# Performance work log

Hardware: AMD Instinct MI355X
Metric: run time of the kernel (lower is better)

## Reference

```python
import jax, jax.numpy as jnp
import numpy as np

SKIP = 2 ** -0.5
EPS = 1e-6
DIM = 1024
N_LAYERS = 8
N_HEADS = 16
MAX_SEQ = 1024
B = 4
L = 1024


def get_rot_emb(dim, max_seq_len):
    pos = jnp.arange(max_seq_len, dtype=jnp.float32)
    omega = 1.0 / 10000.0 ** (jnp.arange(0, dim, 2, dtype=jnp.float32) / dim)
    angles = pos[:, None] * omega[None, :]  # [S, dim/2]
    cos = jnp.repeat(jnp.cos(angles), 2, axis=-1)  # [S, dim]
    sin = jnp.repeat(jnp.sin(angles), 2, axis=-1)
    return cos, sin


def setup_inputs() -> dict:
    key = jax.random.key(0)
    ks = jax.random.split(key, 16)
    s = 0.02
    d = DIM
    nl = N_LAYERS
    cos, sin = get_rot_emb(d // N_HEADS, MAX_SEQ)
    inp = {
        'x': jax.random.normal(ks[0], (B, L, d), jnp.float32),
        'c': jax.random.normal(ks[1], (B, 1, d), jnp.float32),
        't': jax.random.normal(ks[2], (B, d), jnp.float32),
        'num_heads': N_HEADS,
        'cos': cos,
        'sin': sin,
        'qkv_w': jax.random.normal(ks[3], (nl, d, 3 * d), jnp.float32) * s,
        'qkv_b': jnp.zeros((nl, 3 * d), jnp.float32),
        'proj_w': jax.random.normal(ks[4], (nl, d, d), jnp.float32) * s,
        'proj_b': jnp.zeros((nl, d), jnp.float32),
        'mlp_w1': jax.random.normal(ks[5], (nl, d, 4 * d), jnp.float32) * s,
        'mlp_b1': jnp.zeros((nl, 4 * d), jnp.float32),
        'mlp_w2': jax.random.normal(ks[6], (nl, 4 * d, d), jnp.float32) * s,
        'mlp_b2': jnp.zeros((nl, d), jnp.float32),
        'adaln_w': jax.random.normal(ks[7], (nl, d, 6 * d), jnp.float32) * s,
        'adaln_b': jnp.zeros((nl, 6 * d), jnp.float32),
    }
    return inp


def layer_norm(x):
    mu = jnp.mean(x, axis=-1, keepdims=True)
    var = jnp.var(x, axis=-1, keepdims=True)
    return (x - mu) * jax.lax.rsqrt(var + EPS)


def rotate_half(q):
    # torch: stack([-q[..., 1::2], q[..., ::2]], -1).reshape(q.shape)
    q2 = q.reshape(q.shape[:-1] + (-1, 2))
    return jnp.stack([-q2[..., 1], q2[..., 0]], axis=-1).reshape(q.shape)


def reference(x, c, t, num_heads, cos, sin, qkv_w, qkv_b, proj_w, proj_b, mlp_w1, mlp_b1, mlp_w2, mlp_b2, adaln_w, adaln_b):
    Bx, Lx, C = x.shape
    H = int(num_heads)
    D = C // H
    scale = D ** -0.5
    cmod = (c + t[:, None]) * SKIP  # [B,1,C]
    cos_l = cos[:Lx]  # [L,D]
    sin_l = sin[:Lx]

    def block(xcur, p):
        qw, qb, pw, pb, w1, b1, w2, b2, aw, ab = p
        mod = jax.nn.silu(cmod) @ aw + ab  # [B,1,6C]
        sh1, sc1, g1, sh2, sc2, g2 = jnp.split(mod, 6, axis=-1)
        h = (layer_norm(xcur) * (1 + sc1) + sh1) * SKIP
        qkv = (h @ qw + qb).reshape(Bx, Lx, 3, H, D).transpose(2, 0, 3, 1, 4)
        q, k, v = qkv[0], qkv[1], qkv[2]  # [B,H,L,D]
        q = q * cos_l + rotate_half(q) * sin_l
        k = k * cos_l + rotate_half(k) * sin_l
        attn = jax.nn.softmax(scale * jnp.einsum('bhid,bhjd->bhij', q, k), axis=-1)
        o = jnp.einsum('bhij,bhjd->bhid', attn, v).transpose(0, 2, 1, 3).reshape(Bx, Lx, C)
        o = o @ pw + pb
        xcur = (xcur + g1 * o) * SKIP
        h2 = (layer_norm(xcur) * (1 + sc2) + sh2) * SKIP
        m = jax.nn.gelu(h2 @ w1 + b1, approximate=True) @ w2 + b2
        return (xcur + g2 * m) * SKIP, None

    params = (qkv_w, qkv_b, proj_w, proj_b, mlp_w1, mlp_b1, mlp_w2, mlp_b2, adaln_w, adaln_b)
    out, _ = jax.lax.scan(block, x, params)
    return out
```

## Files before the change

kernel.cpp:

```cpp
#include <hip/hip_runtime.h>

#define SKIPF 0.70710678118654752440f

typedef unsigned short u16;
typedef unsigned int u32;
typedef __attribute__((ext_vector_type(4))) short bf16x4;
typedef __attribute__((ext_vector_type(8))) short bf16x8;
typedef __attribute__((ext_vector_type(4))) float f32x4;

#define MFMA32(A, B, C) __builtin_amdgcn_mfma_f32_16x16x32_bf16(A, B, C, 0, 0, 0)
#define MFMA16(A, B, C) __builtin_amdgcn_mfma_f32_16x16x16bf16_1k(A, B, C, 0, 0, 0)

__device__ __forceinline__ float bf2f(u16 v) {
  u32 u = ((u32)v) << 16; float f; __builtin_memcpy(&f, &u, 4); return f;
}
__device__ __forceinline__ u16 f2bf(float f) {
  u32 u; __builtin_memcpy(&u, &f, 4);
  u = (u + 0x7fffu + ((u >> 16) & 1u)) >> 16;
  return (u16)u;
}
__device__ __forceinline__ u32 cvtpk(float a, float b) {
  u32 r;
  asm("v_cvt_pk_bf16_f32 %0, %1, %2" : "=v"(r) : "v"(a), "v"(b));
  return r;
}
__device__ __forceinline__ void gload16(const void* g, void* s) {
  __builtin_amdgcn_global_load_lds((const __attribute__((address_space(1))) void*)g,
                                   (__attribute__((address_space(3))) void*)s, 16, 0, 0);
}

__global__ __launch_bounds__(256) void adaln_part_kernel(const float* __restrict__ c,
                                                         const float* __restrict__ t,
                                                         const float* __restrict__ aw,
                                                         float* __restrict__ part) {
  __shared__ float sc[4][32];
  int n = blockIdx.x * 256 + threadIdx.x;
  int ks = blockIdx.y;
  int k0 = ks * 32;
  if (threadIdx.x < 128) {
    int b = threadIdx.x >> 5, kk = threadIdx.x & 31;
    float xx = (c[b * 1024 + k0 + kk] + t[b * 1024 + k0 + kk]) * SKIPF;
    sc[b][kk] = xx / (1.f + __expf(-xx));
  }
  __syncthreads();
  float a0 = 0.f, a1 = 0.f, a2 = 0.f, a3 = 0.f;
#pragma unroll 4
  for (int k = 0; k < 32; ++k) {
    float w = aw[(size_t)(k0 + k) * 6144 + n];
    a0 += sc[0][k] * w; a1 += sc[1][k] * w; a2 += sc[2][k] * w; a3 += sc[3][k] * w;
  }
  part[(size_t)(ks * 4 + 0) * 6144 + n] = a0;
  part[(size_t)(ks * 4 + 1) * 6144 + n] = a1;
  part[(size_t)(ks * 4 + 2) * 6144 + n] = a2;
  part[(size_t)(ks * 4 + 3) * 6144 + n] = a3;
}

__global__ void adaln_reduce_kernel(const float* __restrict__ part, const float* __restrict__ ab,
                                    float* __restrict__ mod) {
  int i = blockIdx.x * 256 + threadIdx.x;
  int b = i / 6144, n = i - b * 6144;
  float a = ab[n];
#pragma unroll 4
  for (int ks = 0; ks < 32; ++ks) a += part[(size_t)(ks * 4 + b) * 6144 + n];
  mod[(size_t)b * 6144 + n] = a;
}

__global__ void wtrans4_kernel(const float* __restrict__ wq, u16* __restrict__ oq,
                               const float* __restrict__ wp, u16* __restrict__ op,
                               const float* __restrict__ w1p, u16* __restrict__ o1,
                               const float* __restrict__ w2p, u16* __restrict__ o2) {
  __shared__ float tile[32][33];
  int bid = blockIdx.x;
  const float* W; u16* WT; int nx, K, N, base;
  if (bid < 3072)      { W = wq;  WT = oq; nx = 96;  K = 1024; N = 3072; base = 0; }
  else if (bid < 4096) { W = wp;  WT = op; nx = 32;  K = 1024; N = 1024; base = 3072; }
  else if (bid < 8192) { W = w1p; WT = o1; nx = 128; K = 1024; N = 4096; base = 4096; }
  else                 { W = w2p; WT = o2; nx = 32;  K = 4096; N = 1024; base = 8192; }
  int t = bid - base;
  int n0 = (t % nx) * 32, k0 = (t / nx) * 32;
  int tx = threadIdx.x, ty = threadIdx.y;
#pragma unroll
  for (int i = 0; i < 4; ++i)
    tile[ty * 4 + i][tx] = W[(size_t)(k0 + ty * 4 + i) * N + n0 + tx];
  __syncthreads();
#pragma unroll
  for (int i = 0; i < 4; ++i)
    WT[(size_t)(n0 + ty * 4 + i) * K + k0 + tx] = f2bf(tile[tx][ty * 4 + i]);
}

__global__ __launch_bounds__(256) void ln_mod_kernel(const float* __restrict__ xin,
                                                     const float* __restrict__ mod,
                                                     u16* __restrict__ h, int sh_off, int sc_off) {
  int row = blockIdx.x;
  int b = row >> 10;
  const float4* xr = (const float4*)(xin + (size_t)row * 1024);
  float4 v = xr[threadIdx.x];
  float s = v.x + v.y + v.z + v.w;
  float ss = v.x * v.x + v.y * v.y + v.z * v.z + v.w * v.w;
#pragma unroll
  for (int o = 32; o; o >>= 1) { s += __shfl_xor(s, o); ss += __shfl_xor(ss, o); }
  __shared__ float red[8];
  int wave = threadIdx.x >> 6;
  if ((threadIdx.x & 63) == 0) { red[wave * 2] = s; red[wave * 2 + 1] = ss; }
  __syncthreads();
  s = red[0] + red[2] + red[4] + red[6];
  ss = red[1] + red[3] + red[5] + red[7];
  float mu = s * (1.f / 1024.f);
  float var = ss * (1.f / 1024.f) - mu * mu;
  float rs = rsqrtf(var + 1e-6f);
  int n = threadIdx.x * 4;
  const float* mb = mod + (size_t)b * 6144;
  float4 sc = *(const float4*)(mb + sc_off + n);
  float4 sh = *(const float4*)(mb + sh_off + n);
  ushort4 o4;
  o4.x = f2bf(((v.x - mu) * rs * (1.f + sc.x) + sh.x) * SKIPF);
  o4.y = f2bf(((v.y - mu) * rs * (1.f + sc.y) + sh.y) * SKIPF);
  o4.z = f2bf(((v.z - mu) * rs * (1.f + sc.z) + sh.z) * SKIPF);
  o4.w = f2bf(((v.w - mu) * rs * (1.f + sc.w) + sh.w) * SKIPF);
  *(ushort4*)(h + (size_t)row * 1024 + n) = o4;
}

template <int EPI>
__global__ __launch_bounds__(512, 1) void gemm256r_kernel(
    const u16* __restrict__ A, const u16* __restrict__ BT, const float* __restrict__ bias,
    u16* __restrict__ Cb, int NBX, int N, int K) {
  __shared__ u16 lds[4][16384];
  const int tid = threadIdx.x;
  const int lane = tid & 63, wave = tid >> 6;
  const int lq = lane & 15, lk = lane >> 4;
  const int wr = wave >> 2, wc = wave & 3;

  int per = gridDim.x >> 3;
  int swz = (blockIdx.x & 7) * per + (blockIdx.x >> 3);
  int bx = swz % NBX, by = swz / NBX;
  const int m0 = by * 256, n0 = bx * 256;

  f32x4 acc[8][4];
#pragma unroll
  for (int i = 0; i < 8; ++i)
#pragma unroll
    for (int j = 0; j < 4; ++j) acc[i][j] = (f32x4){0.f, 0.f, 0.f, 0.f};

  auto STAGE = [&](int slot, int t) {
    int kt = t * 32;
    char* Ab = (char*)lds[slot];
    char* Bb = (char*)(lds[slot] + 8192);
#pragma unroll
    for (int q = 0; q < 2; ++q) {
      int u = tid + q * 512;
      int r = u >> 3, cpos = u & 7;
      int g = cpos ^ (r & 7);
      gload16(A + (size_t)(m0 + 2 * r + (g >> 2)) * K + kt + (g & 3) * 8, Ab + u * 16);
    }
#pragma unroll
    for (int q = 0; q < 2; ++q) {
      int u = tid + q * 512;
      int r = u >> 3, cpos = u & 7;
      int g = cpos ^ (r & 7);
      gload16(BT + (size_t)(n0 + 2 * r + (g >> 2)) * K + kt + (g & 3) * 8, Bb + u * 16);
    }
  };

  const int NT = K >> 5;
  STAGE(0, 0); STAGE(1, 1); STAGE(2, 2);
  int slot = 0;
  for (int t = 0; t < NT; ++t) {
    int rem = NT - 1 - t;
    if (rem >= 2) asm volatile("s_waitcnt vmcnt(8)" ::: "memory");
    else if (rem == 1) asm volatile("s_waitcnt vmcnt(4)" ::: "memory");
    else asm volatile("s_waitcnt vmcnt(0)" ::: "memory");
    __builtin_amdgcn_s_barrier();
    __builtin_amdgcn_sched_barrier(0);
    if (t + 3 < NT) { int ns = slot + 3; if (ns >= 4) ns -= 4; STAGE(ns, t + 3); }
    const char* Ab = (const char*)lds[slot];
    const char* Bb = (const char*)(lds[slot] + 8192);
    bf16x8 bfr[4];
#pragma unroll
    for (int ni = 0; ni < 4; ++ni) {
      int nrow = wc * 64 + ni * 16 + lq;
      int r = nrow >> 1, g = (nrow & 1) * 4 + lk;
      bfr[ni] = *(const bf16x8*)(Bb + r * 128 + ((g ^ (r & 7)) << 4));
    }
#pragma unroll
    for (int ph = 0; ph < 4; ++ph) {
      bf16x8 af0, af1;
      {
        int mrow = wr * 128 + (ph * 2) * 16 + lq;
        int r = mrow >> 1, g = (mrow & 1) * 4 + lk;
        af0 = *(const bf16x8*)(Ab + r * 128 + ((g ^ (r & 7)) << 4));
        mrow += 16;
        r = mrow >> 1; g = (mrow & 1) * 4 + lk;
        af1 = *(const bf16x8*)(Ab + r * 128 + ((g ^ (r & 7)) << 4));
      }
      __builtin_amdgcn_s_setprio(1);
#pragma unroll
      for (int j = 0; j < 4; ++j) acc[ph * 2][j] = MFMA32(af0, bfr[j], acc[ph * 2][j]);
#pragma unroll
      for (int j = 0; j < 4; ++j) acc[ph * 2 + 1][j] = MFMA32(af1, bfr[j], acc[ph * 2 + 1][j]);
      __builtin_amdgcn_s_setprio(0);
    }
    ++slot; if (slot >= 4) slot = 0;
  }

#pragma unroll
  for (int i = 0; i < 8; ++i) {
    int rbase = m0 + wr * 128 + i * 16 + lk * 4;
#pragma unroll
    for (int j = 0; j < 4; ++j) {
      int cg = n0 + wc * 64 + j * 16 + lq;
      float bv = bias[cg];
#pragma unroll
      for (int r = 0; r < 4; ++r) {
        int row = rbase + r;
        float val = acc[i][j][r] + bv;
        if (EPI == 0) {
          Cb[(size_t)row * N + cg] = f2bf(val);
        } else {
          float tt = 0.7978845608028654f * (val + 0.044715f * val * val * val);
          float e = __expf(2.f * tt);
          float th = 1.f - 2.f / (e + 1.f);
          Cb[(size_t)row * N + cg] = f2bf(0.5f * val * (1.f + th));
        }
      }
    }
  }
}

__global__ __launch_bounds__(256) void gemm_res128_kernel(
    const u16* __restrict__ A, const u16* __restrict__ BT, const float* __restrict__ bias,
    const float* __restrict__ xin, float* __restrict__ xout, const float* __restrict__ mod,
    int g_off, int K) {
  __shared__ u16 lds[3][8192];
  const int tid = threadIdx.x;
  const int lane = tid & 63, wave = tid >> 6;
  const int lq = lane & 15, lk = lane >> 4;
  const int wr = wave >> 1, wc = wave & 1;
  const int m0 = blockIdx.x * 128, n0 = blockIdx.y * 128;

  f32x4 acc[4][4];
#pragma unroll
  for (int i = 0; i < 4; ++i)
#pragma unroll
    for (int j = 0; j < 4; ++j) acc[i][j] = (f32x4){0.f, 0.f, 0.f, 0.f};

  auto STAGE = [&](int slot, int t) {
    int kt = t * 32;
    char* Ab = (char*)lds[slot];
    char* Bb = (char*)(lds[slot] + 4096);
#pragma unroll
    for (int q = 0; q < 2; ++q) {
      int u = tid + q * 256;
      int r = u >> 3, cpos = u & 7;
      int g = cpos ^ (r & 7);
      gload16(A + (size_t)(m0 + 2 * r + (g >> 2)) * K + kt + (g & 3) * 8, Ab + u * 16);
      gload16(BT + (size_t)(n0 + 2 * r + (g >> 2)) * K + kt + (g & 3) * 8, Bb + u * 16);
    }
  };

  const int NT = K >> 5;
  STAGE(0, 0); STAGE(1, 1);
  int slot = 0;
  for (int t = 0; t < NT; ++t) {
    if (t + 1 < NT) asm volatile("s_waitcnt vmcnt(4)" ::: "memory");
    else asm volatile("s_waitcnt vmcnt(0)" ::: "memory");
    __builtin_amdgcn_s_barrier();
    __builtin_amdgcn_sched_barrier(0);
    if (t + 2 < NT) { int ns = slot + 2; if (ns >= 3) ns -= 3; STAGE(ns, t + 2); }
    const char* Ab = (const char*)lds[slot];
    const char* Bb = (const char*)(lds[slot] + 4096);
    bf16x8 af[4], bfr[4];
#pragma unroll
    for (int i = 0; i < 4; ++i) {
      int mrow = wr * 64 + i * 16 + lq;
      int r = mrow >> 1, g = (mrow & 1) * 4 + lk;
      af[i] = *(const bf16x8*)(Ab + r * 128 + ((g ^ (r & 7)) << 4));
    }
#pragma unroll
    for (int j = 0; j < 4; ++j) {
      int nrow = wc * 64 + j * 16 + lq;
      int r = nrow >> 1, g = (nrow & 1) * 4 + lk;
      bfr[j] = *(const bf16x8*)(Bb + r * 128 + ((g ^ (r & 7)) << 4));
    }
    __builtin_amdgcn_s_setprio(1);
#pragma unroll
    for (int i = 0; i < 4; ++i)
#pragma unroll
      for (int j = 0; j < 4; ++j) acc[i][j] = MFMA32(af[i], bfr[j], acc[i][j]);
    __builtin_amdgcn_s_setprio(0);
    ++slot; if (slot >= 3) slot = 0;
  }

#pragma unroll
  for (int i = 0; i < 4; ++i) {
    int rbase = m0 + wr * 64 + i * 16 + lk * 4;
#pragma unroll
    for (int j = 0; j < 4; ++j) {
      int cg = n0 + wc * 64 + j * 16 + lq;
      float bv = bias[cg];
#pragma unroll
      for (int r = 0; r < 4; ++r) {
        int row = rbase + r;
        float val = acc[i][j][r] + bv;
        int b = row >> 10;
        float g = mod[(size_t)b * 6144 + g_off + cg];
        float xv = xin[(size_t)row * 1024 + cg];
        xout[(size_t)row * 1024 + cg] = (xv + g * val) * SKIPF;
      }
    }
  }
}

__global__ __launch_bounds__(256) void ropev_kernel(
    const u16* __restrict__ qkv, const float* __restrict__ cosb, const float* __restrict__ sinb,
    u16* __restrict__ qo, u16* __restrict__ ko, u16* __restrict__ vt) {
  __shared__ u16 tile[64][72];
  int bh = blockIdx.y, l0 = blockIdx.x * 64;
  int b = bh >> 4, h = bh & 15;
  int r = threadIdx.x >> 2, c = (threadIdx.x & 3) * 16;
  int l = l0 + r;
  const u16* src = qkv + (size_t)(b * 1024 + l) * 3072 + h * 64 + c;
  *(uint4*)&tile[r][c] = *(const uint4*)(src + 2048);
  *(uint4*)&tile[r][c + 8] = *(const uint4*)(src + 2048 + 8);
  size_t dst_off = ((size_t)bh * 1024 + l) * 64 + c;
#pragma unroll
  for (int qk = 0; qk < 2; ++qk) {
    const u16* s2 = src + qk * 1024;
    float fs = qk ? 1.f : 0.125f;
    u32 w0[4], w1[4];
#pragma unroll
    for (int p = 0; p < 8; ++p) {
      u32 pr = *(const u32*)(s2 + p * 2);
      int d0 = c + p * 2;
      float cc = cosb[l * 64 + d0], sn = sinb[l * 64 + d0];
      float e0 = bf2f((u16)(pr & 0xffff)), e1 = bf2f((u16)(pr >> 16));
      u32 ow = cvtpk((e0 * cc - e1 * sn) * fs, (e1 * cc + e0 * sn) * fs);
      if (p < 4) w0[p] = ow; else w1[p - 4] = ow;
    }
    u16* dst = (qk ? ko : qo) + dst_off;
    uint4 v0; v0.x = w0[0]; v0.y = w0[1]; v0.z = w0[2]; v0.w = w0[3];
    uint4 v1; v1.x = w1[0]; v1.y = w1[1]; v1.z = w1[2]; v1.w = w1[3];
    *(uint4*)dst = v0;
    *(uint4*)(dst + 8) = v1;
  }
  __syncthreads();
  int d = threadIdx.x >> 2, lc = threadIdx.x & 3;
  u16 tmp[16];
#pragma unroll
  for (int j = 0; j < 16; ++j) tmp[j] = tile[lc * 16 + j][d];
  u16* dstv = vt + ((size_t)bh * 64 + d) * 1024 + l0 + lc * 16;
  *(uint4*)dstv = *(uint4*)tmp;
  *(uint4*)(dstv + 8) = *(uint4*)(tmp + 8);
}

__global__ __launch_bounds__(256) void attn_kernel(const u16* __restrict__ qb,
                                                   const u16* __restrict__ kb,
                                                   const u16* __restrict__ vt,
                                                   u16* __restrict__ ob) {
  __shared__ u16 ktile[3][4096];
  __shared__ u16 vtile[3][4096];
  int nid = (blockIdx.x & 7) * 64 + (blockIdx.x >> 3);
  int qt = nid & 7, bh = nid >> 3;
  int tid = threadIdx.x;
  int lane = tid & 63, wave = tid >> 6;
  int lq = lane & 15, lk = lane >> 4;
  const u16* Q = qb + (size_t)bh * 65536;
  const u16* Kp = kb + (size_t)bh * 65536;
  const u16* VT = vt + (size_t)bh * 65536;
  int qbase = qt * 128 + wave * 32;

  bf16x8 qf[2][2];
#pragma unroll
  for (int g = 0; g < 2; ++g) {
    qf[g][0] = *(const bf16x8*)(Q + (size_t)(qbase + g * 16 + lq) * 64 + lk * 8);
    qf[g][1] = *(const bf16x8*)(Q + (size_t)(qbase + g * 16 + lq) * 64 + 32 + lk * 8);
  }

  auto stage_one = [&](int buf, int kvb, int u) {
    int r = u >> 3;
    int cc = ((u & 7) ^ (r & 7)) * 8;
    gload16(Kp + (size_t)(kvb + r) * 64 + cc, (char*)ktile[buf] + u * 16);
    gload16(VT + (size_t)r * 1024 + kvb + cc, (char*)vtile[buf] + u * 16);
  };

  float mrun[2] = {-1e30f, -1e30f}, lsum[2] = {0.f, 0.f};
  f32x4 oacc[2][4];
#pragma unroll
  for (int g = 0; g < 2; ++g)
#pragma unroll
    for (int f = 0; f < 4; ++f) oacc[g][f] = (f32x4){0.f, 0.f, 0.f, 0.f};
  const f32x4 z4 = (f32x4){0.f, 0.f, 0.f, 0.f};

  stage_one(0, 0, tid); stage_one(0, 0, tid + 256);
  stage_one(1, 64, tid); stage_one(1, 64, tid + 256);
  int slot = 0;
  for (int t = 0; t < 16; ++t) {
    if (t < 15) asm volatile("s_waitcnt vmcnt(4)" ::: "memory");
    else asm volatile("s_waitcnt vmcnt(0)" ::: "memory");
    __builtin_amdgcn_s_barrier();
    __builtin_amdgcn_sched_barrier(0);
    if (t + 2 < 16) {
      int ns = slot + 2; if (ns >= 3) ns -= 3;
      stage_one(ns, (t + 2) * 64, tid);
      stage_one(ns, (t + 2) * 64, tid + 256);
    }
    const char* kb_ = (const char*)ktile[slot];
    const char* vb_ = (const char*)vtile[slot];
    f32x4 st[2][4];
    __builtin_amdgcn_s_setprio(1);
#pragma unroll
    for (int s = 0; s < 4; ++s) {
      int r = s * 16 + lq;
      int sw = (r & 7) << 4;
      bf16x8 kf0 = *(const bf16x8*)(kb_ + r * 128 + ((lk * 16) ^ sw));
      bf16x8 kf1 = *(const bf16x8*)(kb_ + r * 128 + ((64 + lk * 16) ^ sw));
      st[0][s] = MFMA32(kf0, qf[0][0], z4);
      st[0][s] = MFMA32(kf1, qf[0][1], st[0][s]);
      st[1][s] = MFMA32(kf0, qf[1][0], z4);
      st[1][s] = MFMA32(kf1, qf[1][1], st[1][s]);
    }
    __builtin_amdgcn_s_setprio(0);
    bf16x4 pf[2][4];
#pragma unroll
    for (int g = 0; g < 2; ++g) {
      float pm = -1e30f;
#pragma unroll
      for (int s = 0; s < 4; ++s)
#pragma unroll
        for (int r = 0; r < 4; ++r) pm = fmaxf(pm, st[g][s][r]);
      pm = fmaxf(pm, __shfl_xor(pm, 16));
      pm = fmaxf(pm, __shfl_xor(pm, 32));
      if (!__all(pm - mrun[g] <= 8.f)) {
        float mnew = fmaxf(mrun[g], pm);
        float corr = __expf(mrun[g] - mnew);
        float c0 = __shfl(corr, lk * 4 + 0), c1 = __shfl(corr, lk * 4 + 1);
        float c2 = __shfl(corr, lk * 4 + 2), c3 = __shfl(corr, lk * 4 + 3);
#pragma unroll
        for (int f = 0; f < 4; ++f) {
          oacc[g][f][0] *= c0; oacc[g][f][1] *= c1;
          oacc[g][f][2] *= c2; oacc[g][f][3] *= c3;
        }
        lsum[g] *= corr;
        mrun[g] = mnew;
      }
      float ps = 0.f;
#pragma unroll
      for (int s = 0; s < 4; ++s) {
        float p0 = __expf(st[g][s][0] - mrun[g]);
        float p1 = __expf(st[g][s][1] - mrun[g]);
        float p2 = __expf(st[g][s][2] - mrun[g]);
        float p3 = __expf(st[g][s][3] - mrun[g]);
        ps += p0 + p1 + p2 + p3;
        union { bf16x4 v; u32 w[2]; } pu;
        pu.w[0] = cvtpk(p0, p1);
        pu.w[1] = cvtpk(p2, p3);
        pf[g][s] = pu.v;
      }
      ps += __shfl_xor(ps, 16);
      ps += __shfl_xor(ps, 32);
      lsum[g] += ps;
    }
    __builtin_amdgcn_s_setprio(1);
#pragma unroll
    for (int f = 0; f < 4; ++f) {
      int r = lq + f * 16;
      int sw = (r & 7) << 4;
#pragma unroll
      for (int s = 0; s < 4; ++s) {
        bf16x4 vf = *(const bf16x4*)(vb_ + r * 128 + ((s * 32 + lk * 8) ^ sw));
        oacc[0][f] = MFMA16(pf[0][s], vf, oacc[0][f]);
        oacc[1][f] = MFMA16(pf[1][s], vf, oacc[1][f]);
      }
    }
    __builtin_amdgcn_s_setprio(0);
    ++slot; if (slot >= 3) slot = 0;
  }

  int b = bh >> 4, hh = bh & 15;
#pragma unroll
  for (int g = 0; g < 2; ++g) {
    float inv = 1.f / lsum[g];
    float i0 = __shfl(inv, lk * 4 + 0), i1 = __shfl(inv, lk * 4 + 1);
    float i2 = __shfl(inv, lk * 4 + 2), i3 = __shfl(inv, lk * 4 + 3);
#pragma unroll
    for (int f = 0; f < 4; ++f) {
#pragma unroll
      for (int j = 0; j < 4; ++j) {
        int qrow = qbase + g * 16 + lk * 4 + j;
        float sc = (j == 0) ? i0 : (j == 1) ? i1 : (j == 2) ? i2 : i3;
        ob[((size_t)(b * 1024 + qrow)) * 1024 + hh * 64 + lq + f * 16] = f2bf(oacc[g][f][j] * sc);
      }
    }
  }
}


extern "C" void kernel_launch(void* const* d_in, const int* in_sizes, int n_in,
                              void* d_out, int out_size, void* d_ws, size_t ws_size,
                              hipStream_t stream) {
  const float* x = (const float*)d_in[0];
  const float* c = (const float*)d_in[1];
  const float* t = (const float*)d_in[2];
  const float* cosb = (const float*)d_in[4];
  const float* sinb = (const float*)d_in[5];
  const float* qkv_w = (const float*)d_in[6];
  const float* qkv_b = (const float*)d_in[7];
  const float* proj_w = (const float*)d_in[8];
  const float* proj_b = (const float*)d_in[9];
  const float* w1 = (const float*)d_in[10];
  const float* b1 = (const float*)d_in[11];
  const float* w2 = (const float*)d_in[12];
  const float* b2 = (const float*)d_in[13];
  const float* aw = (const float*)d_in[14];
  const float* ab = (const float*)d_in[15];

  constexpr size_t OFF_X = 0;
  constexpr size_t OFF_H = OFF_X + 16777216;
  constexpr size_t OFF_BIG = OFF_H + 8388608;
  constexpr size_t OFF_Q = OFF_BIG + 33554432;
  constexpr size_t OFF_K = OFF_Q + 8388608;
  constexpr size_t OFF_V = OFF_K + 8388608;
  constexpr size_t OFF_AO = OFF_V + 8388608;
  constexpr size_t OFF_WQ = OFF_AO + 8388608;
  constexpr size_t OFF_WP = OFF_WQ + 6291456;
  constexpr size_t OFF_W1 = OFF_WP + 2097152;
  constexpr size_t OFF_W2 = OFF_W1 + 8388608;
  constexpr size_t OFF_MOD = OFF_W2 + 8388608;
  constexpr size_t OFF_PART = OFF_MOD + 98304;

  char* ws = (char*)d_ws;
  float* x_cur = (float*)(ws + OFF_X);
  u16* h = (u16*)(ws + OFF_H);
  u16* big = (u16*)(ws + OFF_BIG);
  u16* qv = (u16*)(ws + OFF_Q);
  u16* kv = (u16*)(ws + OFF_K);
  u16* vt = (u16*)(ws + OFF_V);
  u16* ao = (u16*)(ws + OFF_AO);
  u16* wTq = (u16*)(ws + OFF_WQ);
  u16* wTp = (u16*)(ws + OFF_WP);
  u16* wT1 = (u16*)(ws + OFF_W1);
  u16* wT2 = (u16*)(ws + OFF_W2);
  float* mod = (float*)(ws + OFF_MOD);
  float* part = (float*)(ws + OFF_PART);

  for (int L = 0; L < 8; ++L) {
    const float* awL = aw + (size_t)L * 1024 * 6144;
    const float* abL = ab + (size_t)L * 6144;
    const float* qwL = qkv_w + (size_t)L * 1024 * 3072;
    const float* qbL = qkv_b + (size_t)L * 3072;
    const float* pwL = proj_w + (size_t)L * 1024 * 1024;
    const float* pbL = proj_b + (size_t)L * 1024;
    const float* w1L = w1 + (size_t)L * 1024 * 4096;
    const float* b1L = b1 + (size_t)L * 4096;
    const float* w2L = w2 + (size_t)L * 4096 * 1024;
    const float* b2L = b2 + (size_t)L * 1024;

    const float* xin = (L == 0) ? x : x_cur;
    float* xout2 = (L == 7) ? (float*)d_out : x_cur;

    adaln_part_kernel<<<dim3(24, 32), 256, 0, stream>>>(c, t, awL, part);
    adaln_reduce_kernel<<<96, 256, 0, stream>>>(part, abL, mod);
    wtrans4_kernel<<<12288, dim3(32, 8), 0, stream>>>(qwL, wTq, pwL, wTp, w1L, wT1, w2L, wT2);

    ln_mod_kernel<<<4096, 256, 0, stream>>>(xin, mod, h, 0, 1024);
    gemm256r_kernel<0><<<192, 512, 0, stream>>>(h, wTq, qbL, big, 12, 3072, 1024);
    ropev_kernel<<<dim3(16, 64), 256, 0, stream>>>(big, cosb, sinb, qv, kv, vt);
    attn_kernel<<<512, 256, 0, stream>>>(qv, kv, vt, ao);
    gemm_res128_kernel<<<dim3(32, 8), 256, 0, stream>>>(ao, wTp, pbL, xin, x_cur, mod, 2048, 1024);
    ln_mod_kernel<<<4096, 256, 0, stream>>>(x_cur, mod, h, 3072, 4096);
    gemm256r_kernel<1><<<256, 512, 0, stream>>>(h, wT1, b1L, big, 16, 4096, 1024);
    gemm_res128_kernel<<<dim3(32, 8), 256, 0, stream>>>(big, wT2, b2L, x_cur, xout2, mod, 5120, 4096);
  }
}
```

Baseline: 1.867 ms.

## Halve attention query tile per block and switch KV staging to double buffering

Each attention block now handles 64 query rows instead of 128, with each wave processing 16 rows instead of 32, and the grid doubles to 1024 blocks. The K/V shared-memory pipeline drops from triple to double buffering with a full vmcnt(0) wait each iteration, which lowers LDS use per block. The aim is more blocks and higher occupancy on the many CUs. In exchange, each K/V tile loaded into shared memory is reused by half as many query rows, so global traffic for K/V doubles, and the shallower prefetch exposes more load latency.

```diff
diff --git a/kernel.cpp b/kernel.cpp
--- a/kernel.cpp
+++ b/kernel.cpp
@@ -356,24 +356,20 @@
                                                    const u16* __restrict__ kb,
                                                    const u16* __restrict__ vt,
                                                    u16* __restrict__ ob) {
-  __shared__ u16 ktile[3][4096];
-  __shared__ u16 vtile[3][4096];
-  int nid = (blockIdx.x & 7) * 64 + (blockIdx.x >> 3);
-  int qt = nid & 7, bh = nid >> 3;
+  __shared__ u16 ktile[2][4096];
+  __shared__ u16 vtile[2][4096];
+  int nid = (blockIdx.x & 7) * 128 + (blockIdx.x >> 3);
+  int qt = nid & 15, bh = nid >> 4;
   int tid = threadIdx.x;
   int lane = tid & 63, wave = tid >> 6;
   int lq = lane & 15, lk = lane >> 4;
   const u16* Q = qb + (size_t)bh * 65536;
   const u16* Kp = kb + (size_t)bh * 65536;
   const u16* VT = vt + (size_t)bh * 65536;
-  int qbase = qt * 128 + wave * 32;
-
-  bf16x8 qf[2][2];
-#pragma unroll
-  for (int g = 0; g < 2; ++g) {
-    qf[g][0] = *(const bf16x8*)(Q + (size_t)(qbase + g * 16 + lq) * 64 + lk * 8);
-    qf[g][1] = *(const bf16x8*)(Q + (size_t)(qbase + g * 16 + lq) * 64 + 32 + lk * 8);
-  }
+  int qbase = qt * 64 + wave * 16;
+
+  bf16x8 qf0 = *(const bf16x8*)(Q + (size_t)(qbase + lq) * 64 + lk * 8);
+  bf16x8 qf1 = *(const bf16x8*)(Q + (size_t)(qbase + lq) * 64 + 32 + lk * 8);
 
   auto stage_one = [&](int buf, int kvb, int u) {
     int r = u >> 3;
@@ -382,30 +378,25 @@
     gload16(VT + (size_t)r * 1024 + kvb + cc, (char*)vtile[buf] + u * 16);
   };
 
-  float mrun[2] = {-1e30f, -1e30f}, lsum[2] = {0.f, 0.f};
-  f32x4 oacc[2][4];
-#pragma unroll
-  for (int g = 0; g < 2; ++g)
-#pragma unroll
-    for (int f = 0; f < 4; ++f) oacc[g][f] = (f32x4){0.f, 0.f, 0.f, 0.f};
+  float mrun = -1e30f, lsum = 0.f;
+  f32x4 oacc[4];
+#pragma unroll
+  for (int f = 0; f < 4; ++f) oacc[f] = (f32x4){0.f, 0.f, 0.f, 0.f};
   const f32x4 z4 = (f32x4){0.f, 0.f, 0.f, 0.f};
 
   stage_one(0, 0, tid); stage_one(0, 0, tid + 256);
-  stage_one(1, 64, tid); stage_one(1, 64, tid + 256);
   int slot = 0;
   for (int t = 0; t < 16; ++t) {
-    if (t < 15) asm volatile("s_waitcnt vmcnt(4)" ::: "memory");
-    else asm volatile("s_waitcnt vmcnt(0)" ::: "memory");
+    asm volatile("s_waitcnt vmcnt(0)" ::: "memory");
     __builtin_amdgcn_s_barrier();
     __builtin_amdgcn_sched_barrier(0);
-    if (t + 2 < 16) {
-      int ns = slot + 2; if (ns >= 3) ns -= 3;
-      stage_one(ns, (t + 2) * 64, tid);
-      stage_one(ns, (t + 2) * 64, tid + 256);
+    if (t + 1 < 16) {
+      stage_one(slot ^ 1, (t + 1) * 64, tid);
+      stage_one(slot ^ 1, (t + 1) * 64, tid + 256);
     }
     const char* kb_ = (const char*)ktile[slot];
     const char* vb_ = (const char*)vtile[slot];
-    f32x4 st[2][4];
+    f32x4 st[4];
     __builtin_amdgcn_s_setprio(1);
 #pragma unroll
     for (int s = 0; s < 4; ++s) {
@@ -413,52 +404,47 @@
       int sw = (r & 7) << 4;
       bf16x8 kf0 = *(const bf16x8*)(kb_ + r * 128 + ((lk * 16) ^ sw));
       bf16x8 kf1 = *(const bf16x8*)(kb_ + r * 128 + ((64 + lk * 16) ^ sw));
-      st[0][s] = MFMA32(kf0, qf[0][0], z4);
-      st[0][s] = MFMA32(kf1, qf[0][1], st[0][s]);
-      st[1][s] = MFMA32(kf0, qf[1][0], z4);
-      st[1][s] = MFMA32(kf1, qf[1][1], st[1][s]);
+      st[s] = MFMA32(kf0, qf0, z4);
+      st[s] = MFMA32(kf1, qf1, st[s]);
     }
     __builtin_amdgcn_s_setprio(0);
-    bf16x4 pf[2][4];
-#pragma unroll
-    for (int g = 0; g < 2; ++g) {
-      float pm = -1e30f;
-#pragma unroll
-      for (int s = 0; s < 4; ++s)
-#pragma unroll
-        for (int r = 0; r < 4; ++r) pm = fmaxf(pm, st[g][s][r]);
-      pm = fmaxf(pm, __shfl_xor(pm, 16));
-      pm = fmaxf(pm, __shfl_xor(pm, 32));
-      if (!__all(pm - mrun[g] <= 8.f)) {
-        float mnew = fmaxf(mrun[g], pm);
-        float corr = __expf(mrun[g] - mnew);
-        float c0 = __shfl(corr, lk * 4 + 0), c1 = __shfl(corr, lk * 4 + 1);
-        float c2 = __shfl(corr, lk * 4 + 2), c3 = __shfl(corr, lk * 4 + 3);
-#pragma unroll
-        for (int f = 0; f < 4; ++f) {
-          oacc[g][f][0] *= c0; oacc[g][f][1] *= c1;
-          oacc[g][f][2] *= c2; oacc[g][f][3] *= c3;
-        }
-        lsum[g] *= corr;
-        mrun[g] = mnew;
+    float pm = -1e30f;
+#pragma unroll
+    for (int s = 0; s < 4; ++s)
+#pragma unroll
+      for (int r = 0; r < 4; ++r) pm = fmaxf(pm, st[s][r]);
+    pm = fmaxf(pm, __shfl_xor(pm, 16));
+    pm = fmaxf(pm, __shfl_xor(pm, 32));
+    if (!__all(pm - mrun <= 8.f)) {
+      float mnew = fmaxf(mrun, pm);
+      float corr = __expf(mrun - mnew);
+      float c0 = __shfl(corr, lk * 4 + 0), c1 = __shfl(corr, lk * 4 + 1);
+      float c2 = __shfl(corr, lk * 4 + 2), c3 = __shfl(corr, lk * 4 + 3);
+#pragma unroll
+      for (int f = 0; f < 4; ++f) {
+        oacc[f][0] *= c0; oacc[f][1] *= c1;
+        oacc[f][2] *= c2; oacc[f][3] *= c3;
       }
-      float ps = 0.f;
-#pragma unroll
-      for (int s = 0; s < 4; ++s) {
-        float p0 = __expf(st[g][s][0] - mrun[g]);
-        float p1 = __expf(st[g][s][1] - mrun[g]);
-        float p2 = __expf(st[g][s][2] - mrun[g]);
-        float p3 = __expf(st[g][s][3] - mrun[g]);
-        ps += p0 + p1 + p2 + p3;
-        union { bf16x4 v; u32 w[2]; } pu;
-        pu.w[0] = cvtpk(p0, p1);
-        pu.w[1] = cvtpk(p2, p3);
-        pf[g][s] = pu.v;
-      }
-      ps += __shfl_xor(ps, 16);
-      ps += __shfl_xor(ps, 32);
-      lsum[g] += ps;
-    }
+      lsum *= corr;
+      mrun = mnew;
+    }
+    bf16x4 pf[4];
+    float ps = 0.f;
+#pragma unroll
+    for (int s = 0; s < 4; ++s) {
+      float p0 = __expf(st[s][0] - mrun);
+      float p1 = __expf(st[s][1] - mrun);
+      float p2 = __expf(st[s][2] - mrun);
+      float p3 = __expf(st[s][3] - mrun);
+      ps += p0 + p1 + p2 + p3;
+      union { bf16x4 v; u32 w[2]; } pu;
+      pu.w[0] = cvtpk(p0, p1);
+      pu.w[1] = cvtpk(p2, p3);
+      pf[s] = pu.v;
+    }
+    ps += __shfl_xor(ps, 16);
+    ps += __shfl_xor(ps, 32);
+    lsum += ps;
     __builtin_amdgcn_s_setprio(1);
 #pragma unroll
     for (int f = 0; f < 4; ++f) {
@@ -467,28 +453,24 @@
 #pragma unroll
       for (int s = 0; s < 4; ++s) {
         bf16x4 vf = *(const bf16x4*)(vb_ + r * 128 + ((s * 32 + lk * 8) ^ sw));
-        oacc[0][f] = MFMA16(pf[0][s], vf, oacc[0][f]);
-        oacc[1][f] = MFMA16(pf[1][s], vf, oacc[1][f]);
+        oacc[f] = MFMA16(pf[s], vf, oacc[f]);
       }
     }
     __builtin_amdgcn_s_setprio(0);
-    ++slot; if (slot >= 3) slot = 0;
+    slot ^= 1;
   }
 
   int b = bh >> 4, hh = bh & 15;
-#pragma unroll
-  for (int g = 0; g < 2; ++g) {
-    float inv = 1.f / lsum[g];
-    float i0 = __shfl(inv, lk * 4 + 0), i1 = __shfl(inv, lk * 4 + 1);
-    float i2 = __shfl(inv, lk * 4 + 2), i3 = __shfl(inv, lk * 4 + 3);
-#pragma unroll
-    for (int f = 0; f < 4; ++f) {
-#pragma unroll
-      for (int j = 0; j < 4; ++j) {
-        int qrow = qbase + g * 16 + lk * 4 + j;
-        float sc = (j == 0) ? i0 : (j == 1) ? i1 : (j == 2) ? i2 : i3;
-        ob[((size_t)(b * 1024 + qrow)) * 1024 + hh * 64 + lq + f * 16] = f2bf(oacc[g][f][j] * sc);
-      }
+  float inv = 1.f / lsum;
+  float i0 = __shfl(inv, lk * 4 + 0), i1 = __shfl(inv, lk * 4 + 1);
+  float i2 = __shfl(inv, lk * 4 + 2), i3 = __shfl(inv, lk * 4 + 3);
+#pragma unroll
+  for (int f = 0; f < 4; ++f) {
+#pragma unroll
+    for (int j = 0; j < 4; ++j) {
+      int qrow = qbase + lk * 4 + j;
+      float sc = (j == 0) ? i0 : (j == 1) ? i1 : (j == 2) ? i2 : i3;
+      ob[((size_t)(b * 1024 + qrow)) * 1024 + hh * 64 + lq + f * 16] = f2bf(oacc[f][j] * sc);
     }
   }
 }
@@ -564,7 +546,7 @@
     ln_mod_kernel<<<4096, 256, 0, stream>>>(xin, mod, h, 0, 1024);
     gemm256r_kernel<0><<<192, 512, 0, stream>>>(h, wTq, qbL, big, 12, 3072, 1024);
     ropev_kernel<<<dim3(16, 64), 256, 0, stream>>>(big, cosb, sinb, qv, kv, vt);
-    attn_kernel<<<512, 256, 0, stream>>>(qv, kv, vt, ao);
+    attn_kernel<<<1024, 256, 0, stream>>>(qv, kv, vt, ao);
     gemm_res128_kernel<<<dim3(32, 8), 256, 0, stream>>>(ao, wTp, pbL, xin, x_cur, mod, 2048, 1024);
     ln_mod_kernel<<<4096, 256, 0, stream>>>(x_cur, mod, h, 3072, 4096);
     gemm256r_kernel<1><<<256, 512, 0, stream>>>(h, wT1, b1L, big, 16, 4096, 1024);
```

After: 1.867 ms. No clear change (+0.0%).
